# Kernel tuning notes

Hardware: AMD Instinct MI355X
Metric: run time of the kernel (lower is better)

The kernel has to match this reference:

```python
import jax, jax.numpy as jnp
import numpy as np

N_NODES = 50000
N_EDGES = 1600000
NFEAT = 512
HIDDEN = 128
NUM_CLASSES = 40
DROPOUT = 0.5


def setup_inputs() -> dict:
    key = jax.random.key(0)
    ks = jax.random.split(key, 8)
    x = jax.random.normal(ks[0], (N_NODES, NFEAT), dtype=jnp.float32)
    edge_row = jax.random.randint(ks[1], (N_EDGES,), 0, N_NODES, dtype=jnp.int32)
    edge_col = jax.random.randint(ks[2], (N_EDGES,), 0, N_NODES, dtype=jnp.int32)
    edge_vals = jax.random.uniform(ks[3], (N_EDGES,), dtype=jnp.float32)
    # uniform(-stdv, stdv) init as in reset_parameters
    stdv1 = 1.0 / np.sqrt(HIDDEN)
    stdv2 = 1.0 / np.sqrt(NUM_CLASSES)
    W1 = jax.random.uniform(ks[4], (NFEAT, HIDDEN), dtype=jnp.float32, minval=-stdv1, maxval=stdv1)
    b1 = jax.random.uniform(ks[5], (HIDDEN,), dtype=jnp.float32, minval=-stdv1, maxval=stdv1)
    W2 = jax.random.uniform(ks[6], (HIDDEN, NUM_CLASSES), dtype=jnp.float32, minval=-stdv2, maxval=stdv2)
    b2 = jax.random.uniform(ks[7], (NUM_CLASSES,), dtype=jnp.float32, minval=-stdv2, maxval=stdv2)
    return {"x": x, "edge_row": edge_row, "edge_col": edge_col, "edge_vals": edge_vals,
            "W1": W1, "b1": b1, "W2": W2, "b2": b2}


def _spmm(edge_row, edge_col, edge_vals, support):
    # out[i] = sum_{e: row[e]==i} vals[e] * support[col[e]]  (sparse adj @ support)
    msgs = support[edge_col] * edge_vals[:, None]  # [E, F]
    return jax.ops.segment_sum(msgs, edge_row, num_segments=N_NODES)


def _dropout(x, rate, key):
    keep = 1.0 - rate
    mask = jax.random.bernoulli(key, keep, x.shape)
    return jnp.where(mask, x / keep, jnp.zeros((), x.dtype))


def reference(x, edge_row, edge_col, edge_vals, W1, b1, W2, b2):
    # layer 1: GCN conv + bias + relu + dropout (training=True)
    h = _spmm(edge_row, edge_col, edge_vals, x @ W1) + b1  # [N, H]
    h = jax.nn.relu(h)
    h = _dropout(h, DROPOUT, jax.random.key(42))
    # layer 2: GCN conv + bias + relu
    out = _spmm(edge_row, edge_col, edge_vals, h @ W2) + b2  # [N, C]
    return jax.nn.relu(out)
```

## Files before the change

### kernel.cpp

```cpp
#include <hip/hip_runtime.h>
#include <hip/hip_bf16.h>

#define N_NODES 50000
#define N_EDGES 1600000
#define NFEAT   512
#define HIDDEN  128
#define NCLASS  40

#define NBUCK 391
#define ROWS_PER_BUCKET 128

#define HISTB 782
#define W1T_BLOCKS 256
#define GEMM1_BLOCKS 391
#define PART_T 4096
#define PART_BLOCKS 391

typedef short short8 __attribute__((ext_vector_type(8)));
typedef float f32x4  __attribute__((ext_vector_type(4)));

__device__ __forceinline__ unsigned short f2bu(float f) {
  __hip_bfloat16 h = __float2bfloat16(f);
  return *reinterpret_cast<unsigned short*>(&h);
}

__device__ __forceinline__ unsigned rotl32(unsigned x, int n) {
  return (x << n) | (x >> (32 - n));
}

__device__ __forceinline__ unsigned threefry_bits(unsigned x1) {
  unsigned x0 = 0u;
  const unsigned ks0 = 0u, ks1 = 42u, ks2 = 0x1BD11BDAu ^ 42u;
  x0 += ks0; x1 += ks1;
#define TFR(r) { x0 += x1; x1 = rotl32(x1, (r)); x1 ^= x0; }
  TFR(13) TFR(15) TFR(26) TFR(6)
  x0 += ks1; x1 += ks2 + 1u;
  TFR(17) TFR(29) TFR(16) TFR(24)
  x0 += ks2; x1 += ks0 + 2u;
  TFR(13) TFR(15) TFR(26) TFR(6)
  x0 += ks0; x1 += ks1 + 3u;
  TFR(17) TFR(29) TFR(16) TFR(24)
  x0 += ks1; x1 += ks2 + 4u;
  TFR(13) TFR(15) TFR(26) TFR(6)
  x0 += ks2; x1 += ks0 + 5u;
#undef TFR
  return x0 ^ x1;
}

__global__ __launch_bounds__(256) void hist_w1t_kernel(
    const int* __restrict__ erow, int* __restrict__ bcnt,
    const float* __restrict__ W1, unsigned short* __restrict__ W1T) {
  if (blockIdx.x < HISTB) {
    __shared__ int lcnt[NBUCK];
    const int t = threadIdx.x;
    if (t < NBUCK) lcnt[t] = 0;
    if (t + 256 < NBUCK) lcnt[t + 256] = 0;
    __syncthreads();
    const int base = blockIdx.x * 2048;
#pragma unroll
    for (int k = 0; k < 8; k++) {
      int idx = base + k * 256 + t;
      if (idx < N_EDGES) atomicAdd(&lcnt[erow[idx] >> 7], 1);
    }
    __syncthreads();
    if (t < NBUCK && lcnt[t]) atomicAdd(&bcnt[t], lcnt[t]);
    if (t + 256 < NBUCK && lcnt[t + 256])
      atomicAdd(&bcnt[t + 256], lcnt[t + 256]);
  } else {
    int id = (blockIdx.x - HISTB) * 256 + threadIdx.x;
    int n = id & 127, k = id >> 7;
    W1T[n * NFEAT + k] = f2bu(W1[k * HIDDEN + n]);
  }
}

__device__ __forceinline__ void gemm1_body(
    int bid, const float* __restrict__ x,
    const unsigned short* __restrict__ W1T,
    unsigned short* __restrict__ support) {
  __shared__ short8 As[512];
  __shared__ short8 Bs[512];
  const int t = threadIdx.x;
  const int lane = t & 63;
  const int w = t >> 6;
  const int quad = lane >> 4;
  const int l15 = lane & 15;
  const int node_base = bid * 128;
  const int mbase = (w >> 1) * 64;
  const int nbase = (w & 1) * 64;

  f32x4 acc[4][4] = {};

  for (int k0 = 0; k0 < NFEAT; k0 += 32) {
#pragma unroll
    for (int i = 0; i < 2; i++) {
      int lin = i * 256 + t;
      int n = lin >> 2, q = lin & 3;
      int row = node_base + n;
      if (row >= N_NODES) row = N_NODES - 1;
      const float* src = &x[(size_t)row * NFEAT + k0 + q * 8];
      float4 a = *(const float4*)src;
      float4 b = *(const float4*)(src + 4);
      short8 p;
      p[0] = (short)f2bu(a.x); p[1] = (short)f2bu(a.y);
      p[2] = (short)f2bu(a.z); p[3] = (short)f2bu(a.w);
      p[4] = (short)f2bu(b.x); p[5] = (short)f2bu(b.y);
      p[6] = (short)f2bu(b.z); p[7] = (short)f2bu(b.w);
      As[q * 128 + n] = p;
      Bs[q * 128 + n] = *(const short8*)&W1T[(size_t)n * NFEAT + k0 + q * 8];
    }
    __syncthreads();
    short8 af[4], bfr[4];
#pragma unroll
    for (int mt = 0; mt < 4; mt++)
      af[mt] = As[quad * 128 + mbase + mt * 16 + l15];
#pragma unroll
    for (int nt = 0; nt < 4; nt++)
      bfr[nt] = Bs[quad * 128 + nbase + nt * 16 + l15];
#pragma unroll
    for (int mt = 0; mt < 4; mt++)
#pragma unroll
      for (int nt = 0; nt < 4; nt++)
        acc[mt][nt] = __builtin_amdgcn_mfma_f32_16x16x32_bf16(
            af[mt], bfr[nt], acc[mt][nt], 0, 0, 0);
    __syncthreads();
  }

#pragma unroll
  for (int mt = 0; mt < 4; mt++)
#pragma unroll
    for (int nt = 0; nt < 4; nt++)
#pragma unroll
      for (int r = 0; r < 4; r++) {
        int row = node_base + mbase + mt * 16 + quad * 4 + r;
        int col = nbase + nt * 16 + l15;
        if (row < N_NODES)
          support[(size_t)row * HIDDEN + col] = f2bu(acc[mt][nt][r]);
      }
}

__global__ __launch_bounds__(256) void scan_gemm1_kernel(
    const int* __restrict__ bcnt, int* __restrict__ bbase,
    int* __restrict__ gcur, const float* __restrict__ x,
    const unsigned short* __restrict__ W1T,
    unsigned short* __restrict__ support) {
  if (blockIdx.x == 0) {
    __shared__ int ssc[512];
    const int t = threadIdx.x;
    int c0 = (t < NBUCK) ? bcnt[t] : 0;
    int c1 = (t + 256 < NBUCK) ? bcnt[t + 256] : 0;
    ssc[t] = c0; ssc[t + 256] = c1;
    __syncthreads();
#pragma unroll
    for (int off = 1; off < 512; off <<= 1) {
      int v0 = (t >= off) ? ssc[t - off] : 0;
      int v1 = ssc[t + 256 - off];
      __syncthreads();
      ssc[t] += v0; ssc[t + 256] += v1;
      __syncthreads();
    }
    if (t < NBUCK) { int e = ssc[t] - c0; bbase[t] = e; gcur[t] = e; }
    if (t + 256 < NBUCK) {
      int e = ssc[t + 256] - c1; bbase[t + 256] = e; gcur[t + 256] = e;
    }
    if (t == 0) bbase[NBUCK] = N_EDGES;
  } else {
    gemm1_body(blockIdx.x - 1, x, W1T, support);
  }
}

__global__ __launch_bounds__(256) void partition_kernel(
    const int* __restrict__ erow, const int* __restrict__ ecol,
    const float* __restrict__ evals, int* __restrict__ gcur,
    uint2* __restrict__ eb) {
  __shared__ uint2 sorted[PART_T];
  __shared__ int cnt[NBUCK];
  __shared__ int shift[NBUCK];
  __shared__ int ssc[512];
  const int t = threadIdx.x;
  const int base = blockIdx.x * PART_T;

  if (t < NBUCK) cnt[t] = 0;
  if (t + 256 < NBUCK) cnt[t + 256] = 0;
  __syncthreads();

  uint2 er[16];
  unsigned short loc[16];
#pragma unroll
  for (int k = 0; k < 16; k++) {
    int idx = base + k * 256 + t;
    if (idx < N_EDGES) {
      int r = erow[idx];
      er[k].y = (unsigned)r;
      er[k].x = (unsigned)ecol[idx] | ((unsigned)f2bu(evals[idx]) << 16);
      loc[k] = (unsigned short)atomicAdd(&cnt[r >> 7], 1);
    } else {
      er[k].y = 0xffffffffu;
    }
  }
  __syncthreads();

  ssc[t] = (t < NBUCK) ? cnt[t] : 0;
  ssc[t + 256] = (t + 256 < NBUCK) ? cnt[t + 256] : 0;
  __syncthreads();
#pragma unroll
  for (int off = 1; off < 512; off <<= 1) {
    int v0 = (t >= off) ? ssc[t - off] : 0;
    int v1 = ssc[t + 256 - off];
    __syncthreads();
    ssc[t] += v0; ssc[t + 256] += v1;
    __syncthreads();
  }

  for (int b = t; b < NBUCK; b += 256) {
    int c = cnt[b];
    if (c > 0) {
      int lb = ssc[b] - c;
      int gb = atomicAdd(&gcur[b], c);
      shift[b] = gb - lb;
    }
  }
#pragma unroll
  for (int k = 0; k < 16; k++) {
    if (er[k].y != 0xffffffffu) {
      int b = (int)(er[k].y >> 7);
      sorted[ssc[b] - cnt[b] + (int)loc[k]] = er[k];
    }
  }
  __syncthreads();

  const int total = ssc[NBUCK - 1];
  for (int i = t; i < total; i += 256) {
    uint2 e = sorted[i];
    eb[shift[e.y >> 7] + i] = e;
  }
}

__global__ __launch_bounds__(256) void csr_build_kernel(
    const uint2* __restrict__ eb, const int* __restrict__ bbase,
    unsigned* __restrict__ csr, int* __restrict__ rowptr) {
  __shared__ int cnt[ROWS_PER_BUCKET];
  __shared__ int sc[ROWS_PER_BUCKET];
  __shared__ int cur[ROWS_PER_BUCKET];
  const int t = threadIdx.x;
  const int b = blockIdx.x;
  if (t < ROWS_PER_BUCKET) cnt[t] = 0;
  __syncthreads();
  const int beg = bbase[b], end = bbase[b + 1];
  for (int j = beg + t; j < end; j += 256)
    atomicAdd(&cnt[eb[j].y & 127u], 1);
  __syncthreads();
  if (t < ROWS_PER_BUCKET) sc[t] = cnt[t];
  __syncthreads();
#pragma unroll
  for (int off = 1; off < ROWS_PER_BUCKET; off <<= 1) {
    int v = 0;
    if (t >= off && t < ROWS_PER_BUCKET) v = sc[t - off];
    __syncthreads();
    if (t < ROWS_PER_BUCKET) sc[t] += v;
    __syncthreads();
  }
  if (t < ROWS_PER_BUCKET) {
    int excl = sc[t] - cnt[t];
    cur[t] = excl;
    int row = b * ROWS_PER_BUCKET + t;
    if (row < N_NODES) rowptr[row] = beg + excl;
    if (row == N_NODES - 1) rowptr[N_NODES] = N_EDGES;
  }
  __syncthreads();
  for (int j = beg + t; j < end; j += 256) {
    uint2 e = eb[j];
    int p = atomicAdd(&cur[e.y & 127u], 1);
    csr[beg + p] = e.x;
  }
}

__global__ __launch_bounds__(256) void spmm1_fused(
    const unsigned* __restrict__ csr, const int* __restrict__ rowptr,
    const unsigned* __restrict__ sup,
    const float* __restrict__ b1, unsigned* __restrict__ h) {
  const int row = blockIdx.x * 4 + (threadIdx.x >> 6);
  const int lane = threadIdx.x & 63;
  const int beg = rowptr[row], end = rowptr[row + 1];
  float ax = 0.f, ay = 0.f;
  int j = beg;
  for (; j + 7 < end; j += 8) {
    unsigned p0 = csr[j],     p1 = csr[j + 1], p2 = csr[j + 2], p3 = csr[j + 3];
    unsigned p4 = csr[j + 4], p5 = csr[j + 5], p6 = csr[j + 6], p7 = csr[j + 7];
    unsigned u0 = sup[(p0 & 0xffffu) * 64 + lane];
    unsigned u1 = sup[(p1 & 0xffffu) * 64 + lane];
    unsigned u2 = sup[(p2 & 0xffffu) * 64 + lane];
    unsigned u3 = sup[(p3 & 0xffffu) * 64 + lane];
    unsigned u4 = sup[(p4 & 0xffffu) * 64 + lane];
    unsigned u5 = sup[(p5 & 0xffffu) * 64 + lane];
    unsigned u6 = sup[(p6 & 0xffffu) * 64 + lane];
    unsigned u7 = sup[(p7 & 0xffffu) * 64 + lane];
    float v0 = __uint_as_float(p0 & 0xffff0000u);
    float v1 = __uint_as_float(p1 & 0xffff0000u);
    float v2 = __uint_as_float(p2 & 0xffff0000u);
    float v3 = __uint_as_float(p3 & 0xffff0000u);
    float v4 = __uint_as_float(p4 & 0xffff0000u);
    float v5 = __uint_as_float(p5 & 0xffff0000u);
    float v6 = __uint_as_float(p6 & 0xffff0000u);
    float v7 = __uint_as_float(p7 & 0xffff0000u);
    ax += v0 * __uint_as_float(u0 << 16) + v1 * __uint_as_float(u1 << 16) +
          v2 * __uint_as_float(u2 << 16) + v3 * __uint_as_float(u3 << 16) +
          v4 * __uint_as_float(u4 << 16) + v5 * __uint_as_float(u5 << 16) +
          v6 * __uint_as_float(u6 << 16) + v7 * __uint_as_float(u7 << 16);
    ay += v0 * __uint_as_float(u0 & 0xffff0000u) +
          v1 * __uint_as_float(u1 & 0xffff0000u) +
          v2 * __uint_as_float(u2 & 0xffff0000u) +
          v3 * __uint_as_float(u3 & 0xffff0000u) +
          v4 * __uint_as_float(u4 & 0xffff0000u) +
          v5 * __uint_as_float(u5 & 0xffff0000u) +
          v6 * __uint_as_float(u6 & 0xffff0000u) +
          v7 * __uint_as_float(u7 & 0xffff0000u);
  }
  for (; j + 1 < end; j += 2) {
    unsigned p0 = csr[j], p1 = csr[j + 1];
    unsigned u0 = sup[(p0 & 0xffffu) * 64 + lane];
    unsigned u1 = sup[(p1 & 0xffffu) * 64 + lane];
    float v0 = __uint_as_float(p0 & 0xffff0000u);
    float v1 = __uint_as_float(p1 & 0xffff0000u);
    ax += v0 * __uint_as_float(u0 << 16) + v1 * __uint_as_float(u1 << 16);
    ay += v0 * __uint_as_float(u0 & 0xffff0000u) +
          v1 * __uint_as_float(u1 & 0xffff0000u);
  }
  if (j < end) {
    unsigned p0 = csr[j];
    unsigned u0 = sup[(p0 & 0xffffu) * 64 + lane];
    float v0 = __uint_as_float(p0 & 0xffff0000u);
    ax += v0 * __uint_as_float(u0 << 16);
    ay += v0 * __uint_as_float(u0 & 0xffff0000u);
  }
  const unsigned i0 = (unsigned)row * HIDDEN + lane * 2;
  float vx = fmaxf(ax + b1[lane * 2], 0.f);
  float vy = fmaxf(ay + b1[lane * 2 + 1], 0.f);
  vx = (threefry_bits(i0) >> 31) ? 0.f : 2.f * vx;
  vy = (threefry_bits(i0 + 1) >> 31) ? 0.f : 2.f * vy;
  h[(unsigned)row * 64 + lane] = (unsigned)f2bu(vx) | ((unsigned)f2bu(vy) << 16);
}

__global__ __launch_bounds__(256) void gemm2_kernel(
    const uint4* __restrict__ h,
    const float* __restrict__ W2, unsigned short* __restrict__ h2) {
  __shared__ float Hs[64][132];
  __shared__ float Ws[40][132];
  const int t = threadIdx.x;
  const int node_base = blockIdx.x * 64;
#pragma unroll
  for (int i = 0; i < 4; i++) {
    int lin = i * 256 + t;
    int nloc = lin >> 4, c8 = lin & 15;
    int n = node_base + nloc;
    if (n >= N_NODES) n = N_NODES - 1;
    uint4 u = h[(size_t)n * 16 + c8];
    float* d = &Hs[nloc][c8 * 8];
    d[0] = __uint_as_float(u.x << 16); d[1] = __uint_as_float(u.x & 0xffff0000u);
    d[2] = __uint_as_float(u.y << 16); d[3] = __uint_as_float(u.y & 0xffff0000u);
    d[4] = __uint_as_float(u.z << 16); d[5] = __uint_as_float(u.z & 0xffff0000u);
    d[6] = __uint_as_float(u.w << 16); d[7] = __uint_as_float(u.w & 0xffff0000u);
  }
#pragma unroll
  for (int i = 0; i < 20; i++) {
    int l = t + i * 256;
    int k = l / NCLASS, f = l % NCLASS;
    Ws[f][k] = W2[l];
  }
  __syncthreads();
  const int nloc = t >> 2;
  const int fb = t & 3;
  const int n = node_base + nloc;
  float acc[10];
#pragma unroll
  for (int j = 0; j < 10; j++) acc[j] = 0.f;
  for (int k = 0; k < HIDDEN; k += 4) {
    float4 a = *(const float4*)&Hs[nloc][k];
#pragma unroll
    for (int j = 0; j < 10; j++) {
      float4 wv = *(const float4*)&Ws[fb + 4 * j][k];
      acc[j] += a.x * wv.x + a.y * wv.y + a.z * wv.z + a.w * wv.w;
    }
  }
  if (n < N_NODES) {
#pragma unroll
    for (int j = 0; j < 10; j++)
      h2[(size_t)n * NCLASS + fb + 4 * j] = f2bu(acc[j]);
  }
}

__global__ __launch_bounds__(256) void spmm2_fused(
    const unsigned* __restrict__ csr, const int* __restrict__ rowptr,
    const unsigned* __restrict__ h2u,
    const float* __restrict__ b2, float* __restrict__ out) {
  const int row = blockIdx.x * 4 + (threadIdx.x >> 6);
  const int lane = threadIdx.x & 63;
  const int half = lane >> 5;
  const int il = lane & 31;
  const unsigned ilc = (il < 20) ? (unsigned)il : 19u;
  const int beg = rowptr[row], end = rowptr[row + 1];
  float ax = 0.f, ay = 0.f;
  int j = beg + half;
  for (; j + 2 < end; j += 4) {
    unsigned p0 = csr[j];
    unsigned p1 = csr[j + 2];
    unsigned u0 = h2u[(p0 & 0xffffu) * 20 + ilc];
    unsigned u1 = h2u[(p1 & 0xffffu) * 20 + ilc];
    float v0 = __uint_as_float(p0 & 0xffff0000u);
    float v1 = __uint_as_float(p1 & 0xffff0000u);
    ax += v0 * __uint_as_float(u0 << 16) + v1 * __uint_as_float(u1 << 16);
    ay += v0 * __uint_as_float(u0 & 0xffff0000u) +
          v1 * __uint_as_float(u1 & 0xffff0000u);
  }
  for (; j < end; j += 2) {
    unsigned p0 = csr[j];
    unsigned u0 = h2u[(p0 & 0xffffu) * 20 + ilc];
    float v0 = __uint_as_float(p0 & 0xffff0000u);
    ax += v0 * __uint_as_float(u0 << 16);
    ay += v0 * __uint_as_float(u0 & 0xffff0000u);
  }
  ax += __shfl_xor(ax, 32);
  ay += __shfl_xor(ay, 32);
  if (half == 0 && il < 20) {
    float2 r;
    r.x = fmaxf(ax + b2[il * 2], 0.f);
    r.y = fmaxf(ay + b2[il * 2 + 1], 0.f);
    *(float2*)&out[(unsigned)row * NCLASS + il * 2] = r;
  }
}

extern "C" void kernel_launch(void* const* d_in, const int* in_sizes, int n_in,
                              void* d_out, int out_size, void* d_ws,
                              size_t ws_size, hipStream_t stream) {
  const float* x     = (const float*)d_in[0];
  const int*   erow  = (const int*)d_in[1];
  const int*   ecol  = (const int*)d_in[2];
  const float* evals = (const float*)d_in[3];
  const float* W1    = (const float*)d_in[4];
  const float* b1    = (const float*)d_in[5];
  const float* W2    = (const float*)d_in[6];
  const float* b2    = (const float*)d_in[7];
  float* out = (float*)d_out;

  char* base = (char*)d_ws;
  unsigned short* support = (unsigned short*)base;
  uint2*          eb  = (uint2*)(base + 12800000);
  unsigned*       h   = (unsigned*)(base + 12800000);
  unsigned short* h2  = (unsigned short*)(base + 25600000);
  unsigned short* W1T = (unsigned short*)(base + 29600000);
  unsigned*       csr = (unsigned*)(base + 29731072);
  int* rowptr = (int*)(base + 36131072);
  int* bcnt   = rowptr + (N_NODES + 4);
  int* bbase  = bcnt + 400;
  int* gcur   = bbase + 400;

  hipMemsetAsync(bcnt, 0, NBUCK * sizeof(int), stream);

  hist_w1t_kernel<<<HISTB + W1T_BLOCKS, 256, 0, stream>>>(erow, bcnt, W1, W1T);
  scan_gemm1_kernel<<<1 + GEMM1_BLOCKS, 256, 0, stream>>>(
      bcnt, bbase, gcur, x, W1T, support);
  partition_kernel<<<PART_BLOCKS, 256, 0, stream>>>(erow, ecol, evals, gcur,
                                                    eb);
  csr_build_kernel<<<NBUCK, 256, 0, stream>>>(eb, bbase, csr, rowptr);
  spmm1_fused<<<N_NODES / 4, 256, 0, stream>>>(csr, rowptr,
                                               (const unsigned*)support, b1, h);
  gemm2_kernel<<<(N_NODES + 63) / 64, 256, 0, stream>>>((const uint4*)h, W2,
                                                        h2);
  spmm2_fused<<<N_NODES / 4, 256, 0, stream>>>(csr, rowptr,
                                               (const unsigned*)h2, b2, out);
}
```

Before: 365.4 us.

## Co-schedule partition with GEMM1, split scan, widen CSR build and SpMM unroll

Moves the bucket scan into its own single-block kernel and fuses the edge partition with the first dense GEMM into one launch, so the latency-bound partition blocks and the MFMA GEMM blocks run concurrently instead of back to back. The CSR build uses 512-thread blocks, and both SpMM kernels gain deeper unrolled gather loops (16 edges for layer 1, 4 pairs for layer 2) to keep more loads in flight. The combined kernel's shared-memory footprint is the larger of the two bodies, which may reduce occupancy for the GEMM blocks. Wider unrolling also raises register pressure.

```diff
diff --git a/kernel.cpp b/kernel.cpp
--- a/kernel.cpp
+++ b/kernel.cpp
@@ -73,6 +73,30 @@
   }
 }
 
+__global__ __launch_bounds__(256) void scan_kernel(
+    const int* __restrict__ bcnt, int* __restrict__ bbase,
+    int* __restrict__ gcur) {
+  __shared__ int ssc[512];
+  const int t = threadIdx.x;
+  int c0 = (t < NBUCK) ? bcnt[t] : 0;
+  int c1 = (t + 256 < NBUCK) ? bcnt[t + 256] : 0;
+  ssc[t] = c0; ssc[t + 256] = c1;
+  __syncthreads();
+#pragma unroll
+  for (int off = 1; off < 512; off <<= 1) {
+    int v0 = (t >= off) ? ssc[t - off] : 0;
+    int v1 = ssc[t + 256 - off];
+    __syncthreads();
+    ssc[t] += v0; ssc[t + 256] += v1;
+    __syncthreads();
+  }
+  if (t < NBUCK) { int e = ssc[t] - c0; bbase[t] = e; gcur[t] = e; }
+  if (t + 256 < NBUCK) {
+    int e = ssc[t + 256] - c1; bbase[t + 256] = e; gcur[t + 256] = e;
+  }
+  if (t == 0) bbase[NBUCK] = N_EDGES;
+}
+
 __device__ __forceinline__ void gemm1_body(
     int bid, const float* __restrict__ x,
     const unsigned short* __restrict__ W1T,
@@ -138,38 +162,8 @@
       }
 }
 
-__global__ __launch_bounds__(256) void scan_gemm1_kernel(
-    const int* __restrict__ bcnt, int* __restrict__ bbase,
-    int* __restrict__ gcur, const float* __restrict__ x,
-    const unsigned short* __restrict__ W1T,
-    unsigned short* __restrict__ support) {
-  if (blockIdx.x == 0) {
-    __shared__ int ssc[512];
-    const int t = threadIdx.x;
-    int c0 = (t < NBUCK) ? bcnt[t] : 0;
-    int c1 = (t + 256 < NBUCK) ? bcnt[t + 256] : 0;
-    ssc[t] = c0; ssc[t + 256] = c1;
-    __syncthreads();
-#pragma unroll
-    for (int off = 1; off < 512; off <<= 1) {
-      int v0 = (t >= off) ? ssc[t - off] : 0;
-      int v1 = ssc[t + 256 - off];
-      __syncthreads();
-      ssc[t] += v0; ssc[t + 256] += v1;
-      __syncthreads();
-    }
-    if (t < NBUCK) { int e = ssc[t] - c0; bbase[t] = e; gcur[t] = e; }
-    if (t + 256 < NBUCK) {
-      int e = ssc[t + 256] - c1; bbase[t + 256] = e; gcur[t + 256] = e;
-    }
-    if (t == 0) bbase[NBUCK] = N_EDGES;
-  } else {
-    gemm1_body(blockIdx.x - 1, x, W1T, support);
-  }
-}
-
-__global__ __launch_bounds__(256) void partition_kernel(
-    const int* __restrict__ erow, const int* __restrict__ ecol,
+__device__ __forceinline__ void partition_body(
+    int bid, const int* __restrict__ erow, const int* __restrict__ ecol,
     const float* __restrict__ evals, int* __restrict__ gcur,
     uint2* __restrict__ eb) {
   __shared__ uint2 sorted[PART_T];
@@ -177,7 +171,7 @@
   __shared__ int shift[NBUCK];
   __shared__ int ssc[512];
   const int t = threadIdx.x;
-  const int base = blockIdx.x * PART_T;
+  const int base = bid * PART_T;
 
   if (t < NBUCK) cnt[t] = 0;
   if (t + 256 < NBUCK) cnt[t + 256] = 0;
@@ -235,7 +229,19 @@
   }
 }
 
-__global__ __launch_bounds__(256) void csr_build_kernel(
+__global__ __launch_bounds__(256) void part_gemm1_kernel(
+    const int* __restrict__ erow, const int* __restrict__ ecol,
+    const float* __restrict__ evals, int* __restrict__ gcur,
+    uint2* __restrict__ eb, const float* __restrict__ x,
+    const unsigned short* __restrict__ W1T,
+    unsigned short* __restrict__ support) {
+  if (blockIdx.x < PART_BLOCKS)
+    partition_body(blockIdx.x, erow, ecol, evals, gcur, eb);
+  else
+    gemm1_body(blockIdx.x - PART_BLOCKS, x, W1T, support);
+}
+
+__global__ __launch_bounds__(512) void csr_build_kernel(
     const uint2* __restrict__ eb, const int* __restrict__ bbase,
     unsigned* __restrict__ csr, int* __restrict__ rowptr) {
   __shared__ int cnt[ROWS_PER_BUCKET];
@@ -246,7 +252,7 @@
   if (t < ROWS_PER_BUCKET) cnt[t] = 0;
   __syncthreads();
   const int beg = bbase[b], end = bbase[b + 1];
-  for (int j = beg + t; j < end; j += 256)
+  for (int j = beg + t; j < end; j += 512)
     atomicAdd(&cnt[eb[j].y & 127u], 1);
   __syncthreads();
   if (t < ROWS_PER_BUCKET) sc[t] = cnt[t];
@@ -267,7 +273,7 @@
     if (row == N_NODES - 1) rowptr[N_NODES] = N_EDGES;
   }
   __syncthreads();
-  for (int j = beg + t; j < end; j += 256) {
+  for (int j = beg + t; j < end; j += 512) {
     uint2 e = eb[j];
     int p = atomicAdd(&cur[e.y & 127u], 1);
     csr[beg + p] = e.x;
@@ -283,37 +289,31 @@
   const int beg = rowptr[row], end = rowptr[row + 1];
   float ax = 0.f, ay = 0.f;
   int j = beg;
+  for (; j + 15 < end; j += 16) {
+    unsigned p[16], u[16];
+#pragma unroll
+    for (int k = 0; k < 16; k++) p[k] = csr[j + k];
+#pragma unroll
+    for (int k = 0; k < 16; k++) u[k] = sup[(p[k] & 0xffffu) * 64 + lane];
+#pragma unroll
+    for (int k = 0; k < 16; k++) {
+      float v = __uint_as_float(p[k] & 0xffff0000u);
+      ax += v * __uint_as_float(u[k] << 16);
+      ay += v * __uint_as_float(u[k] & 0xffff0000u);
+    }
+  }
   for (; j + 7 < end; j += 8) {
-    unsigned p0 = csr[j],     p1 = csr[j + 1], p2 = csr[j + 2], p3 = csr[j + 3];
-    unsigned p4 = csr[j + 4], p5 = csr[j + 5], p6 = csr[j + 6], p7 = csr[j + 7];
-    unsigned u0 = sup[(p0 & 0xffffu) * 64 + lane];
-    unsigned u1 = sup[(p1 & 0xffffu) * 64 + lane];
-    unsigned u2 = sup[(p2 & 0xffffu) * 64 + lane];
-    unsigned u3 = sup[(p3 & 0xffffu) * 64 + lane];
-    unsigned u4 = sup[(p4 & 0xffffu) * 64 + lane];
-    unsigned u5 = sup[(p5 & 0xffffu) * 64 + lane];
-    unsigned u6 = sup[(p6 & 0xffffu) * 64 + lane];
-    unsigned u7 = sup[(p7 & 0xffffu) * 64 + lane];
-    float v0 = __uint_as_float(p0 & 0xffff0000u);
-    float v1 = __uint_as_float(p1 & 0xffff0000u);
-    float v2 = __uint_as_float(p2 & 0xffff0000u);
-    float v3 = __uint_as_float(p3 & 0xffff0000u);
-    float v4 = __uint_as_float(p4 & 0xffff0000u);
-    float v5 = __uint_as_float(p5 & 0xffff0000u);
-    float v6 = __uint_as_float(p6 & 0xffff0000u);
-    float v7 = __uint_as_float(p7 & 0xffff0000u);
-    ax += v0 * __uint_as_float(u0 << 16) + v1 * __uint_as_float(u1 << 16) +
-          v2 * __uint_as_float(u2 << 16) + v3 * __uint_as_float(u3 << 16) +
-          v4 * __uint_as_float(u4 << 16) + v5 * __uint_as_float(u5 << 16) +
-          v6 * __uint_as_float(u6 << 16) + v7 * __uint_as_float(u7 << 16);
-    ay += v0 * __uint_as_float(u0 & 0xffff0000u) +
-          v1 * __uint_as_float(u1 & 0xffff0000u) +
-          v2 * __uint_as_float(u2 & 0xffff0000u) +
-          v3 * __uint_as_float(u3 & 0xffff0000u) +
-          v4 * __uint_as_float(u4 & 0xffff0000u) +
-          v5 * __uint_as_float(u5 & 0xffff0000u) +
-          v6 * __uint_as_float(u6 & 0xffff0000u) +
-          v7 * __uint_as_float(u7 & 0xffff0000u);
+    unsigned p[8], u[8];
+#pragma unroll
+    for (int k = 0; k < 8; k++) p[k] = csr[j + k];
+#pragma unroll
+    for (int k = 0; k < 8; k++) u[k] = sup[(p[k] & 0xffffu) * 64 + lane];
+#pragma unroll
+    for (int k = 0; k < 8; k++) {
+      float v = __uint_as_float(p[k] & 0xffff0000u);
+      ax += v * __uint_as_float(u[k] << 16);
+      ay += v * __uint_as_float(u[k] & 0xffff0000u);
+    }
   }
   for (; j + 1 < end; j += 2) {
     unsigned p0 = csr[j], p1 = csr[j + 1];
@@ -400,6 +400,19 @@
   const int beg = rowptr[row], end = rowptr[row + 1];
   float ax = 0.f, ay = 0.f;
   int j = beg + half;
+  for (; j + 6 < end; j += 8) {
+    unsigned p[4], u[4];
+#pragma unroll
+    for (int k = 0; k < 4; k++) p[k] = csr[j + 2 * k];
+#pragma unroll
+    for (int k = 0; k < 4; k++) u[k] = h2u[(p[k] & 0xffffu) * 20 + ilc];
+#pragma unroll
+    for (int k = 0; k < 4; k++) {
+      float v = __uint_as_float(p[k] & 0xffff0000u);
+      ax += v * __uint_as_float(u[k] << 16);
+      ay += v * __uint_as_float(u[k] & 0xffff0000u);
+    }
+  }
   for (; j + 2 < end; j += 4) {
     unsigned p0 = csr[j];
     unsigned p1 = csr[j + 2];
@@ -456,11 +469,10 @@
   hipMemsetAsync(bcnt, 0, NBUCK * sizeof(int), stream);
 
   hist_w1t_kernel<<<HISTB + W1T_BLOCKS, 256, 0, stream>>>(erow, bcnt, W1, W1T);
-  scan_gemm1_kernel<<<1 + GEMM1_BLOCKS, 256, 0, stream>>>(
-      bcnt, bbase, gcur, x, W1T, support);
-  partition_kernel<<<PART_BLOCKS, 256, 0, stream>>>(erow, ecol, evals, gcur,
-                                                    eb);
-  csr_build_kernel<<<NBUCK, 256, 0, stream>>>(eb, bbase, csr, rowptr);
+  scan_kernel<<<1, 256, 0, stream>>>(bcnt, bbase, gcur);
+  part_gemm1_kernel<<<PART_BLOCKS + GEMM1_BLOCKS, 256, 0, stream>>>(
+      erow, ecol, evals, gcur, eb, x, W1T, support);
+  csr_build_kernel<<<NBUCK, 512, 0, stream>>>(eb, bbase, csr, rowptr);
   spmm1_fused<<<N_NODES / 4, 256, 0, stream>>>(csr, rowptr,
                                                (const unsigned*)support, b1, h);
   gemm2_kernel<<<(N_NODES + 63) / 64, 256, 0, stream>>>((const uint4*)h, W2,
```

Measured after the change: 349.5 us. 4.3% less time.
